# Kernel optimization log

Measured on AMD Instinct MI355X. Metric: run time of the kernel, lower is better.

The kernel has to match this reference:

```python
import jax, jax.numpy as jnp
import numpy as np

B, L, D_MODEL = 2, 2048, 256
D_STATE, D_CONV, EXPAND, HEADDIM = 128, 4, 4, 64
D_INNER = EXPAND * D_MODEL            # 1024
NHEADS = D_INNER // HEADDIM           # 16
CONV_DIM = D_INNER + 2 * D_STATE      # 1280
D_IN_PROJ = 2 * D_INNER + 2 * D_STATE + NHEADS  # 2320
CHUNK = 256
GN_EPS = float(np.finfo(np.float32).eps)
RMS_EPS = 1e-5


def _silu(x):
    return x * jax.nn.sigmoid(x)


def _segsum(x):
    # x: (..., T) -> (..., T, T); out[i, j] = sum_{j<k<=i} x[k] for i>=j else -inf
    T = x.shape[-1]
    cs = jnp.cumsum(x, -1)
    d = cs[..., :, None] - cs[..., None, :]
    mask = jnp.tril(jnp.ones((T, T), bool))
    return jnp.where(mask, d, -jnp.inf)


def _ssd(X, A, Bm, Cm):
    # Chunked SSD (Mamba2 ssd_minimal_discrete). X:(b,l,h,p) already dt-scaled,
    # A:(b,l,h) = dt * (-exp(A_log)), Bm/Cm:(b,l,n) with ngroups=1.
    b, l, h, p = X.shape
    c = l // CHUNK
    Xc = X.reshape(b, c, CHUNK, h, p)
    Ac = jnp.transpose(A.reshape(b, c, CHUNK, h), (0, 3, 1, 2))  # (b,h,c,Q)
    Bc = Bm.reshape(b, c, CHUNK, -1)
    Cc = Cm.reshape(b, c, CHUNK, -1)
    A_cs = jnp.cumsum(Ac, -1)                                    # (b,h,c,Q)
    Lmat = jnp.exp(_segsum(Ac))                                  # (b,h,c,Q,Q)
    CB = jnp.einsum('bcln,bcsn->bcls', Cc, Bc)                   # (b,c,Q,Q)
    Y_diag = jnp.einsum('bhcls,bcshp->bclhp', Lmat * CB[:, None], Xc)
    decay_states = jnp.exp(A_cs[..., -1:] - A_cs)                # (b,h,c,Q)
    states = jnp.einsum('bcln,bhcl,bclhp->bchpn', Bc, decay_states, Xc)
    states = jnp.concatenate([jnp.zeros_like(states[:, :1]), states], 1)  # (b,c+1,h,p,n)
    decay_chunk = jnp.exp(_segsum(jnp.pad(A_cs[..., -1], ((0, 0), (0, 0), (1, 0)))))  # (b,h,c+1,c+1)
    new_states = jnp.einsum('bhzc,bchpn->bzhpn', decay_chunk, states)[:, :-1]
    state_decay = jnp.exp(A_cs)                                  # (b,h,c,Q)
    Y_off = jnp.einsum('bcln,bchpn,bhcl->bclhp', Cc, new_states, state_decay)
    return (Y_diag + Y_off).reshape(b, l, h, p)


def _mamba2(u, in_w, conv_w, conv_b, dt_bias, A_log, Dh, norm_w, out_w):
    # u: (b, l, d_model)
    b, l, _ = u.shape
    zxbcdt = u @ in_w.T                                          # (b,l,D_IN_PROJ)
    z = zxbcdt[..., :D_INNER]
    xBC = zxbcdt[..., D_INNER:D_INNER + CONV_DIM]
    dt = jax.nn.softplus(zxbcdt[..., -NHEADS:] + dt_bias)        # (b,l,h)
    # causal depthwise conv over time
    xc = jnp.transpose(xBC, (0, 2, 1))                           # (b,C,l)
    xc = jax.lax.conv_general_dilated(xc, conv_w, (1,), [(D_CONV - 1, 0)],
                                      dimension_numbers=('NCH', 'OIH', 'NCH'),
                                      feature_group_count=CONV_DIM)
    xBC = _silu(jnp.transpose(xc + conv_b[None, :, None], (0, 2, 1)))
    x = xBC[..., :D_INNER].reshape(b, l, NHEADS, HEADDIM)
    Bm = xBC[..., D_INNER:D_INNER + D_STATE]
    Cm = xBC[..., D_INNER + D_STATE:]
    A = dt * (-jnp.exp(A_log))                                   # (b,l,h)
    y = _ssd(dt[..., None] * x, A, Bm, Cm) + x * Dh[None, None, :, None]
    y = y.reshape(b, l, D_INNER) * _silu(z)                      # gated
    y = y * jax.lax.rsqrt(jnp.mean(y * y, -1, keepdims=True) + RMS_EPS) * norm_w
    return y @ out_w.T                                           # (b,l,d_model)


def _resmamba(x, gn_w, gn_b, fp, bp, proj_w, proj_b):
    # GroupNorm(1, C) over (C, L) per sample
    mu = jnp.mean(x, (1, 2), keepdims=True)
    var = jnp.mean((x - mu) ** 2, (1, 2), keepdims=True)
    xn = (x - mu) * jax.lax.rsqrt(var + GN_EPS) * gn_w[None, :, None] + gn_b[None, :, None]
    t = jnp.transpose(xn, (0, 2, 1))                             # (B,L,C)
    fwd = _mamba2(t, *fp)
    bwd = jnp.flip(_mamba2(jnp.flip(t, 1), *bp), 1)
    r = jnp.concatenate([fwd + t, bwd + t], -1)                  # (B,L,2C)
    pr = r @ proj_w.T + proj_b                                   # (B,L,C)
    return x + jnp.transpose(pr, (0, 2, 1))


def setup_inputs():
    key = jax.random.key(0)
    ks = jax.random.split(key, 4)
    s = 0.02
    inp = {
        'x': jax.random.normal(ks[0], (B, D_MODEL, L), jnp.float32),
        'gn_w': jnp.ones((D_MODEL,), jnp.float32),
        'gn_b': jnp.zeros((D_MODEL,), jnp.float32),
        'proj_w': s * jax.random.normal(ks[1], (D_MODEL, 2 * D_MODEL), jnp.float32),
        'proj_b': jnp.zeros((D_MODEL,), jnp.float32),
    }
    for i, p in enumerate(('f', 'b')):
        kk = jax.random.split(ks[2 + i], 5)
        inp[p + '_in_w'] = s * jax.random.normal(kk[0], (D_IN_PROJ, D_MODEL), jnp.float32)
        inp[p + '_conv_w'] = s * jax.random.normal(kk[1], (CONV_DIM, 1, D_CONV), jnp.float32)
        inp[p + '_conv_b'] = jnp.zeros((CONV_DIM,), jnp.float32)
        inp[p + '_dt_bias'] = 0.1 * jax.random.normal(kk[2], (NHEADS,), jnp.float32)
        inp[p + '_A_log'] = jnp.log(jax.random.uniform(kk[3], (NHEADS,), jnp.float32, 1.0, 16.0))
        inp[p + '_D'] = jnp.ones((NHEADS,), jnp.float32)
        inp[p + '_norm_w'] = jnp.ones((D_INNER,), jnp.float32)
        inp[p + '_out_w'] = s * jax.random.normal(kk[4], (D_MODEL, D_INNER), jnp.float32)
    return inp


def reference(x, gn_w, gn_b, proj_w, proj_b,
              f_in_w, f_conv_w, f_conv_b, f_dt_bias, f_A_log, f_D, f_norm_w, f_out_w,
              b_in_w, b_conv_w, b_conv_b, b_dt_bias, b_A_log, b_D, b_norm_w, b_out_w):
    fp = (f_in_w, f_conv_w, f_conv_b, f_dt_bias, f_A_log, f_D, f_norm_w, f_out_w)
    bp = (b_in_w, b_conv_w, b_conv_b, b_dt_bias, b_A_log, b_D, b_norm_w, b_out_w)
    return _resmamba(x, gn_w, gn_b, fp, bp, proj_w, proj_b)
```

## Files before the change

### kernel.cpp

```cpp
#include <hip/hip_runtime.h>
#include <hip/hip_bf16.h>
#include <math.h>

using bf16 = __hip_bfloat16;

#define L_SEQ   2048
#define DMODEL  256
#define DINNER  1024
#define DSTATE  128
#define NH      16
#define HD      64
#define CONVDIM 1280
#define DPROJ   2320
#define NCHK    8
#define CT      256
#define BATCH   2
#define M_TOT   (BATCH*L_SEQ)

#define ACS_N   (BATCH*NH*NCHK*CT)
#define ST_N    ((size_t)BATCH*NCHK*NH*HD*DSTATE)
#define CB_N    ((size_t)BATCH*NCHK*CT*CT)

typedef __bf16 bf16x8_t __attribute__((ext_vector_type(8)));
typedef __bf16 bf16x4_t __attribute__((ext_vector_type(4)));
// ... 50 lines not shown
      for (int i = 0; i < 8; ++i) o[i] = tile[kr][j8+i];
      *(bf16x8_t*)&dst[(size_t)(k0+kr)*DMODEL + j0 + j8] = o;
    }
  } else if (bz < 1448){
    int i = ((bz - 1416)*256 + t)*8;
    int j = i & 255;
    const float* row = pw + (size_t)(i >> 8)*(2*DMODEL);
    bf16x8_t o;
    #pragma unroll
    for (int c = 0; c < 8; ++c) o[c] = (__bf16)(row[j+c] + row[256+j+c]);
    *(bf16x8_t*)&psum[i] = o;
  } else {
    int sub = bz - 1448;
    int blk = sub & 127, b = sub >> 7;
    const float4* p = (const float4*)(x + (size_t)b*(DMODEL*L_SEQ) + (size_t)blk*4096);
    float s = 0.f, ss = 0.f;
    #pragma unroll
    for (int k = 0; k < 4; ++k){
      float4 v = p[t + k*256];
      s  += v.x + v.y + v.z + v.w;
      ss += v.x*v.x + v.y*v.y + v.z*v.z + v.w*v.w;
    }
    for (int o = 32; o > 0; o >>= 1){ s += __shfl_down(s, o, 64); ss += __shfl_down(ss, o, 64); }
    if ((t & 63) == 0){ sh[(t>>6)*2] = s; sh[(t>>6)*2+1] = ss; }
    __syncthreads();
    if (t == 0){
      s  = sh[0]+sh[2]+sh[4]+sh[6];
      ss = sh[1]+sh[3]+sh[5]+sh[7];
      pbuf[b*128 + blk] = make_float2(s, ss);
    }
  }
}

__global__ __launch_bounds__(256) void k_t(const float* __restrict__ x, const float* __restrict__ gw,
                                           const float* __restrict__ gb, const float2* __restrict__ pbuf,
                                           bf16* __restrict__ t_out){
  __shared__ float tile[64][65];
  __shared__ float sh[4];
  int l0 = blockIdx.x*64, c0 = blockIdx.y*64, b = blockIdx.z;
  int tid = threadIdx.x;
  float s = 0.f, ss = 0.f;
  if (tid < 128){ float2 v = pbuf[b*128 + tid]; s = v.x; ss = v.y; }
  for (int o = 32; o > 0; o >>= 1){ s += __shfl_down(s, o, 64); ss += __shfl_down(ss, o, 64); }
  if (tid < 128 && (tid & 63) == 0){ sh[(tid>>6)*2] = s; sh[(tid>>6)*2+1] = ss; }
  __syncthreads();
  float inv = 1.f/(float)(DMODEL*L_SEQ);
  float s0 = sh[0]+sh[2], ss0 = sh[1]+sh[3];
  float mu = s0*inv, var = ss0*inv - mu*mu;
  float istd = rsqrtf(fmaxf(var, 0.f) + 1.1920929e-07f);

  int lx = tid & 63, cy = tid >> 6;
  for (int cc = cy; cc < 64; cc += 4){
    float v = x[(size_t)b*DMODEL*L_SEQ + (size_t)(c0+cc)*L_SEQ + l0+lx];
    tile[cc][lx] = (v - mu)*istd;
  }
  __syncthreads();
  int cx = tid & 63, ly = tid >> 6;
  float w = gw[c0+cx], bb = gb[c0+cx];
  for (int ll = ly; ll < 64; ll += 4)
    t_out[((size_t)(b*L_SEQ) + l0+ll)*DMODEL + c0+cx] = tob(tile[cx][ll]*w + bb);
}

__global__ __launch_bounds__(256) void gemm_inproj(const bf16* __restrict__ A, const bf16* __restrict__ B,
                                                   bf16* __restrict__ z, bf16* __restrict__ xbc,
                                                   float* __restrict__ dtb,
                                                   const float* __restrict__ db0, const float* __restrict__ db1){
  __shared__ __align__(16) bf16 lds[2][(128+128)*40];
  const int lda = DMODEL, ldb = DMODEL, N = DPROJ;
  int dir = blockIdx.z;
  const bf16* Bd = B + (size_t)dir*(size_t)N*ldb;
  int orig = blockIdx.x;
  int swz = (orig & 7)*76 + (orig >> 3);
  int m0 = (swz & 31)*128;
  int n0 = (swz >> 5)*128;
  int t = threadIdx.x;
  int wave = t >> 6, lane = t & 63;
  int wm = (wave & 1)*64, wn = (wave >> 1)*64;
  int lrow = lane & 15, quad = lane >> 4, lk8 = quad*8;

  int r0 = t >> 2, o0 = (t & 3)*8;
  int r1 = r0 + 64;
  int am0 = m0 + r0, am1 = m0 + r1;
  if (dir){
    am0 = (am0 & ~(L_SEQ-1)) | ((L_SEQ-1) - (am0 & (L_SEQ-1)));
    am1 = (am1 & ~(L_SEQ-1)) | ((L_SEQ-1) - (am1 & (L_SEQ-1)));
  }
  int bn0 = n0 + r0; if (bn0 > N-1) bn0 = N-1;
  int bn1 = n0 + r1; if (bn1 > N-1) bn1 = N-1;
  const bf16* Ap0 = A + (size_t)am0*lda + o0;
  const bf16* Ap1 = A + (size_t)am1*lda + o0;
  const bf16* Bp0 = Bd + (size_t)bn0*ldb + o0;
  const bf16* Bp1 = Bd + (size_t)bn1*ldb + o0;

  f32x4_t acc[4][4];
  #pragma unroll
  for (int i = 0; i < 4; ++i)
    #pragma unroll
    for (int j = 0; j < 4; ++j) acc[i][j] = (f32x4_t){0,0,0,0};

  int nit = 8;
  uint4 a0 = *(const uint4*)Ap0;
  uint4 a1 = *(const uint4*)Ap1;
  uint4 b0 = *(const uint4*)Bp0;
  uint4 b1 = *(const uint4*)Bp1;
  int st = 0;
  *(uint4*)&lds[0][r0*40 + o0] = a0;
  *(uint4*)&lds[0][r1*40 + o0] = a1;
  *(uint4*)&lds[0][(128 + r0)*40 + o0] = b0;
  *(uint4*)&lds[0][(128 + r1)*40 + o0] = b1;
  __syncthreads();
  for (int it = 0; it < nit; ++it){
    bool more = (it+1 < nit);
    if (more){
      int kk = (it+1) << 5;
      a0 = *(const uint4*)(Ap0 + kk);
      a1 = *(const uint4*)(Ap1 + kk);
      b0 = *(const uint4*)(Bp0 + kk);
      b1 = *(const uint4*)(Bp1 + kk);
    }
    const bf16* cs = lds[st];
    bf16x8_t bfr[4];
    #pragma unroll
    for (int ni = 0; ni < 4; ++ni) bfr[ni] = *(const bf16x8_t*)&cs[(128 + wn + ni*16 + lrow)*40 + lk8];
    #pragma unroll
    for (int mi = 0; mi < 4; ++mi){
      bf16x8_t af = *(const bf16x8_t*)&cs[(wm + mi*16 + lrow)*40 + lk8];
      #pragma unroll
      for (int ni = 0; ni < 4; ++ni)
        acc[mi][ni] = __builtin_amdgcn_mfma_f32_16x16x32_bf16(af, bfr[ni], acc[mi][ni], 0, 0, 0);
    }
    if (more){
      st ^= 1;
      *(uint4*)&lds[st][r0*40 + o0] = a0;
      *(uint4*)&lds[st][r1*40 + o0] = a1;
      *(uint4*)&lds[st][(128 + r0)*40 + o0] = b0;
      *(uint4*)&lds[st][(128 + r1)*40 + o0] = b1;
      __syncthreads();
    }
  }

  if (n0 < DINNER + CONVDIM){
    __syncthreads();
    __bf16* outs = (__bf16*)lds;
    #pragma unroll
    for (int mi = 0; mi < 4; ++mi)
      #pragma unroll
      for (int ni = 0; ni < 4; ++ni)
        #pragma unroll
        for (int r = 0; r < 4; ++r)
          outs[(wm + mi*16 + quad*4 + r)*132 + wn + ni*16 + lrow] = (__bf16)acc[mi][ni][r];
    __syncthreads();
    bf16* dst; int ldd, c0;
    if (n0 < DINNER){ dst = z   + (size_t)dir*M_TOT*DINNER;  ldd = DINNER;  c0 = n0; }
    else            { dst = xbc + (size_t)dir*M_TOT*CONVDIM; ldd = CONVDIM; c0 = n0 - DINNER; }
    #pragma unroll
    for (int itv = 0; itv < 8; ++itv){
      int v = t + itv*256;
      int row = v >> 4, cb = v & 15;
      *(bf16x8_t*)&dst[(size_t)(m0+row)*ldd + c0 + cb*8] =
          *(const bf16x8_t*)&outs[row*132 + cb*8];
    }
  } else {
    const float* db = dir ? db1 : db0;
    float* dtp = dtb + (size_t)dir*((size_t)M_TOT*NH);
    #pragma unroll
    for (int mi = 0; mi < 4; ++mi)
      #pragma unroll
      for (int ni = 0; ni < 4; ++ni)
        #pragma unroll
        for (int r = 0; r < 4; ++r){
          int m = m0 + wm + mi*16 + quad*4 + r;
          int n = n0 + wn + ni*16 + lrow;
          if (n < N){
            int h = n - (DINNER + CONVDIM);
            float xx = acc[mi][ni][r] + db[h];
            dtp[(size_t)m*NH + h] = (xx > 20.f) ? xx : log1pf(expf(xx));
          }
        }
  }
}

__global__ __launch_bounds__(256) void gemm_w(const bf16* __restrict__ P, const bf16* __restrict__ owt,
                                              bf16* __restrict__ W){
  __shared__ __align__(16) bf16 lds[2][(128+64)*40];
  int dir = blockIdx.z;
  int m0 = blockIdx.x*128, n0 = blockIdx.y*64;
  int t = threadIdx.x;
  int wave = t >> 6, lane = t & 63;
  int wm = (wave & 1)*64, wn = (wave >> 1)*32;
  int lrow = lane & 15, quad = lane >> 4, lk8 = quad*8;

  int r0 = t >> 2, o0 = (t & 3)*8;
  int r1 = r0 + 64;
  const bf16* Ap0 = P + (size_t)(m0 + r0)*(2*DMODEL) + dir*DMODEL + o0;
  const bf16* Ap1 = P + (size_t)(m0 + r1)*(2*DMODEL) + dir*DMODEL + o0;
  const bf16* Bp  = owt + (size_t)dir*DINNER*DMODEL + (size_t)(n0 + r0)*DMODEL + o0;

  f32x4_t acc[4][2];
  #pragma unroll
  for (int i = 0; i < 4; ++i){ acc[i][0] = (f32x4_t){0,0,0,0}; acc[i][1] = (f32x4_t){0,0,0,0}; }

  int nit = DMODEL >> 5;
  uint4 a0 = *(const uint4*)Ap0;
  uint4 a1 = *(const uint4*)Ap1;
  uint4 b0 = *(const uint4*)Bp;
  int st = 0;
  *(uint4*)&lds[0][r0*40 + o0] = a0;
  *(uint4*)&lds[0][r1*40 + o0] = a1;
  *(uint4*)&lds[0][(128 + r0)*40 + o0] = b0;
  __syncthreads();
  for (int it = 0; it < nit; ++it){
    bool more = (it+1 < nit);
    if (more){
      int kk = (it+1) << 5;
      a0 = *(const uint4*)(Ap0 + kk);
      a1 = *(const uint4*)(Ap1 + kk);
      b0 = *(const uint4*)(Bp + kk);
    }
    const bf16* cs = lds[st];
    bf16x8_t af[4], bfr[2];
    #pragma unroll
    for (int mi = 0; mi < 4; ++mi) af[mi] = *(const bf16x8_t*)&cs[(wm + mi*16 + lrow)*40 + lk8];
    #pragma unroll
    for (int ni = 0; ni < 2; ++ni) bfr[ni] = *(const bf16x8_t*)&cs[(128 + wn + ni*16 + lrow)*40 + lk8];
    #pragma unroll
    for (int mi = 0; mi < 4; ++mi)
      #pragma unroll
      for (int ni = 0; ni < 2; ++ni)
        acc[mi][ni] = __builtin_amdgcn_mfma_f32_16x16x32_bf16(af[mi], bfr[ni], acc[mi][ni], 0, 0, 0);
    if (more){
      st ^= 1;
      *(uint4*)&lds[st][r0*40 + o0] = a0;
      *(uint4*)&lds[st][r1*40 + o0] = a1;
      *(uint4*)&lds[st][(128 + r0)*40 + o0] = b0;
      __syncthreads();
    }
  }
  bf16* Wd = W + (size_t)dir*DMODEL*DINNER;
  #pragma unroll
  for (int mi = 0; mi < 4; ++mi)
    #pragma unroll
    for (int ni = 0; ni < 2; ++ni)
      #pragma unroll
      for (int r = 0; r < 4; ++r){
        int m = m0 + wm + mi*16 + quad*4 + r;
        int n = n0 + wn + ni*16 + lrow;
        Wd[(size_t)m*DINNER + n] = tob(acc[mi][ni][r]);
      }
}

__global__ __launch_bounds__(256) void gemm_final(const bf16* __restrict__ y, const bf16* __restrict__ tb,
                                                  const bf16* __restrict__ W, const bf16* __restrict__ psum,
                                                  const float* __restrict__ x, const float* __restrict__ pb,
                                                  float* __restrict__ out){
  __shared__ __align__(16) bf16 lds[2][(32+64)*72];
  __shared__ float tile[32][65];
  int orig = blockIdx.x;
  int swz = (orig & 7)*64 + (orig >> 3);
  int mt_ = swz & 127, nt_ = swz >> 7;
  int m0 = mt_*32, n0 = nt_*64;
  int t = threadIdx.x;
  int wave = t >> 6, lane = t & 63;
  int lrow = lane & 15, quad = lane >> 4, lk8 = quad*8;
  int wn = wave*16;

  f32x4_t acc[2];
  acc[0] = (f32x4_t){0,0,0,0}; acc[1] = (f32x4_t){0,0,0,0};

  int rowA = t >> 3, oA = (t & 7)*8;
  int rowB0 = t >> 3, oB0 = (t & 7)*8;
  int rowB1 = (t + 256) >> 3, oB1 = (t & 7)*8;

  #pragma unroll
  for (int ph = 0; ph < 3; ++ph){
    const bf16 *Ab, *Bb; int lda, ldb, K, rev;
    if (ph == 0){ Ab = y;                             lda = DINNER; K = DINNER; Bb = W;                             ldb = DINNER; rev = 0; }
    else if (ph == 1){ Ab = y + (size_t)M_TOT*DINNER; lda = DINNER; K = DINNER; Bb = W + (size_t)DMODEL*DINNER;     ldb = DINNER; rev = 1; }
    else { Ab = tb; lda = DMODEL; K = DMODEL; Bb = psum; ldb = DMODEL; rev = 0; }

    int am = m0 + rowA;
    if (rev) am = (am & ~(L_SEQ-1)) | ((L_SEQ-1) - (am & (L_SEQ-1)));
// ... 89 lines not shown
  {
    float4 b0v = *(const float4*)&cb[ch0];
    float4 b1v = *(const float4*)&cb[ch0+4];
    bias[0]=b0v.x; bias[1]=b0v.y; bias[2]=b0v.z; bias[3]=b0v.w;
    bias[4]=b1v.x; bias[5]=b1v.y; bias[6]=b1v.z; bias[7]=b1v.w;
  }

  bf16x8_t zero;
  #pragma unroll
  for (int c = 0; c < 8; ++c) zero[c] = (__bf16)0.f;

  bf16x8_t win[4];
  #pragma unroll
  for (int k = 0; k < 3; ++k){
    int ls = lbase - 3 + k;
    win[k] = (ls >= 0) ? *(const bf16x8_t*)&xr[(size_t)ls*CONVDIM] : zero;
  }
  #pragma unroll
  for (int i = 0; i < 4; ++i){
    int l = lbase + i;
    win[3] = *(const bf16x8_t*)&xr[(size_t)l*CONVDIM];
    bf16x8_t outv;
    #pragma unroll
    for (int c = 0; c < 8; ++c){
      float a = bias[c] + (float)win[0][c]*wk[0][c] + (float)win[1][c]*wk[1][c]
                        + (float)win[2][c]*wk[2][c] + (float)win[3][c]*wk[3][c];
      outv[c] = (__bf16)(a / (1.f + __expf(-a)));
    }
    *(bf16x8_t*)&xcv[(size_t)l*CONVDIM] = outv;
    win[0] = win[1]; win[1] = win[2]; win[2] = win[3];
  }
}

__global__ __launch_bounds__(256) void k_states(const bf16* __restrict__ xconv, const float* __restrict__ dt,
                                                const float* __restrict__ Al0, const float* __restrict__ Al1,
                                                float* __restrict__ A_cs, float* __restrict__ states){
  int id0 = blockIdx.x;
  int dir = id0 >> 8; int id = id0 & 255;
  int h = id & 15; int bc = id >> 4; int ch = bc & 7; int b = bc >> 3;
  int t = threadIdx.x;
  __shared__ float s_acs[CT];
  __shared__ float w_s[CT];
  __shared__ __align__(16) __bf16 Xt[64*72];
  __shared__ __align__(16) __bf16 Bt[128*72];
  const bf16* xc = xconv + (size_t)dir*((size_t)M_TOT*CONVDIM);
  const float* dtp = dt + (size_t)dir*((size_t)M_TOT*NH);
  const float* Alog = dir ? Al1 : Al0;
  size_t rowbase = (size_t)(b*L_SEQ) + ch*CT;

  float dtv = dtp[(rowbase + t)*NH + h];
  s_acs[t] = -expf(Alog[h]) * dtv;
  __syncthreads();
  for (int off = 1; off < 256; off <<= 1){
    float v = (t >= off) ? s_acs[t-off] : 0.f;
    __syncthreads();
    s_acs[t] += v;
    __syncthreads();
  }
  A_cs[(size_t)dir*ACS_N + (size_t)((b*NH+h)*NCHK + ch)*CT + t] = s_acs[t];
  float alast = s_acs[CT-1];
  w_s[t] = dtv * __expf(fminf(alast - s_acs[t], 0.f));
  __syncthreads();

  int wave = t >> 6, lane = t & 63, lrow = lane & 15, quad = lane >> 4;
  f32x4_t acc[8];
  #pragma unroll
  for (int i = 0; i < 8; ++i) acc[i] = (f32x4_t){0.f,0.f,0.f,0.f};

  for (int kt = 0; kt < 4; ++kt){
    int l0 = kt*64;
    #pragma unroll
    for (int it = 0; it < 2; ++it){
      int idx = t + it*256; int l = idx >> 3; int p0 = (idx & 7)*8;
      bf16x8_t v = *(const bf16x8_t*)&xc[(rowbase + l0 + l)*CONVDIM + h*HD + p0];
      float w = w_s[l0 + l];
      int col = (((l>>3) ^ ((p0>>3)&7))<<3) | (l&7);
      #pragma unroll
      for (int j = 0; j < 8; ++j) Xt[(p0+j)*72 + col] = (__bf16)((float)v[j]*w);
    }
    #pragma unroll
    for (int it = 0; it < 4; ++it){
      int idx = t + it*256; int l = idx >> 4; int n0 = (idx & 15)*8;
      bf16x8_t v = *(const bf16x8_t*)&xc[(rowbase + l0 + l)*CONVDIM + DINNER + n0];
      int col = (((l>>3) ^ ((n0>>3)&7))<<3) | (l&7);
      #pragma unroll
      for (int j = 0; j < 8; ++j) Bt[(n0+j)*72 + col] = v[j];
    }
    __syncthreads();
    int arow = wave*16 + lrow;
    #pragma unroll
    for (int ks = 0; ks < 2; ++ks){
      int kg = ks*4 + quad;
      bf16x8_t af = *(const bf16x8_t*)&Xt[arow*72 + ((kg ^ ((arow>>3)&7))<<3)];
      #pragma unroll
      for (int nt = 0; nt < 8; ++nt){
        int brow = nt*16 + lrow;
        bf16x8_t bq = *(const bf16x8_t*)&Bt[brow*72 + ((kg ^ ((brow>>3)&7))<<3)];
        acc[nt] = __builtin_amdgcn_mfma_f32_16x16x32_bf16(af, bq, acc[nt], 0, 0, 0);
      }
    }
    __syncthreads();
  }
  float* so = states + (size_t)dir*ST_N + (size_t)id*HD*DSTATE;
  int m = wave*16 + quad*4;
  #pragma unroll
  for (int nt = 0; nt < 8; ++nt)
    #pragma unroll
    for (int r = 0; r < 4; ++r)
      so[(size_t)(m+r)*DSTATE + nt*16 + lrow] = acc[nt][r];
}

__global__ __launch_bounds__(256) void k_recur(const float* __restrict__ states, bf16* __restrict__ nsb,
                                               const float* __restrict__ A_cs){
  int blk = blockIdx.x;
  int bh2 = blk >> 5;
  int e = (blk & 31)*256 + threadIdx.x;
  int dir = bh2 >> 5; int bh = bh2 & 31;
  int h = bh & 15, b = bh >> 4;
  const float* ac = A_cs + (size_t)dir*ACS_N;
  const float* st = states + (size_t)dir*ST_N;
  bf16* nb = nsb + (size_t)dir*ST_N;
  float s = 0.f;
  #pragma unroll
  for (int ch = 0; ch < NCHK; ++ch){
    float dec = expdec(ac[((size_t)(bh*NCHK+ch))*CT + CT-1]);
    size_t off = (size_t)(((b*NCHK+ch)*NH)+h)*HD*DSTATE + e;
    float cur = st[off];
    nb[off] = tob(s);
    s = s*dec + cur;
  }
}

__global__ __launch_bounds__(256) void k_cb(const bf16* __restrict__ xconv, bf16* __restrict__ CB){
  int zz = blockIdx.z;
  int dir = zz >> 4; int b = (zz >> 3) & 1; int ch = zz & 7;
  int m0 = blockIdx.x*64, n0 = blockIdx.y*64;
  if (n0 > m0) return;
  const bf16* base = xconv + (size_t)dir*((size_t)M_TOT*CONVDIM) + (size_t)(b*L_SEQ + ch*CT)*CONVDIM;
  const bf16* Crow = base + DINNER + DSTATE;
  const bf16* Brow = base + DINNER;
  __shared__ __align__(16) __bf16 As[64*136];
  __shared__ __align__(16) __bf16 Bs[64*136];
  int t = threadIdx.x;
  int r = t >> 2, o0 = (t & 3)*32;
  #pragma unroll
  for (int j = 0; j < 4; ++j){
    *(bf16x8_t*)&As[r*136 + o0 + j*8] = *(const bf16x8_t*)&Crow[(size_t)(m0+r)*CONVDIM + o0 + j*8];
    *(bf16x8_t*)&Bs[r*136 + o0 + j*8] = *(const bf16x8_t*)&Brow[(size_t)(n0+r)*CONVDIM + o0 + j*8];
  }
  __syncthreads();
  int wave = t >> 6, lane = t & 63, lrow = lane & 15, quad = lane >> 4;
  int wm = wave*16;
  f32x4_t acc[4];
  #pragma unroll
  for (int i = 0; i < 4; ++i) acc[i] = (f32x4_t){0.f,0.f,0.f,0.f};
  #pragma unroll
  for (int ks = 0; ks < 4; ++ks){
    bf16x8_t af = *(const bf16x8_t*)&As[(wm+lrow)*136 + ks*32 + quad*8];
    #pragma unroll
    for (int nt = 0; nt < 4; ++nt){
      bf16x8_t bq = *(const bf16x8_t*)&Bs[(nt*16+lrow)*136 + ks*32 + quad*8];
      acc[nt] = __builtin_amdgcn_mfma_f32_16x16x32_bf16(af, bq, acc[nt], 0, 0, 0);
    }
  }
  __syncthreads();
  #pragma unroll
  for (int nt = 0; nt < 4; ++nt)
    #pragma unroll
    for (int r2 = 0; r2 < 4; ++r2)
      As[(wm + quad*4 + r2)*72 + nt*16 + lrow] = (__bf16)acc[nt][r2];
  __syncthreads();
  bf16* outp = CB + (size_t)dir*CB_N + (size_t)(b*NCHK+ch)*CT*CT;
  #pragma unroll
  for (int p = 0; p < 2; ++p){
    int idx = t + p*256;
    int row = idx >> 3, c8 = (idx & 7)*8;
    *(bf16x8_t*)&outp[(size_t)(m0+row)*CT + n0 + c8] = *(const bf16x8_t*)&As[row*72 + c8];
  }
}

__global__ __launch_bounds__(512) void k_y_mfma(const bf16* __restrict__ xconv, const float* __restrict__ dt,
                                                const float* __restrict__ A_cs, const bf16* __restrict__ CB,
                                                const bf16* __restrict__ ns, bf16* __restrict__ y){
  int id0 = blockIdx.x;
  int dir = id0 >> 8; int id = id0 & 255;
  int h = id & 15; int bc = id >> 4; int ch = bc & 7; int b = bc >> 3;
  int t = threadIdx.x;
  int lane = t & 63;
  int lrow = lane & 15, quad = lane >> 4;

  __shared__ __align__(16) bf16 Xs[64*264];
  __shared__ __align__(16) bf16 NSs[64*136];
  __shared__ float acs_s[CT];

  const bf16* xc = xconv + (size_t)dir*((size_t)M_TOT*CONVDIM);
  const float* dtp = dt + (size_t)dir*((size_t)M_TOT*NH);
  const float* acs = A_cs + (size_t)dir*ACS_N + (size_t)((b*NH+h)*NCHK + ch)*CT;
  const bf16* cbz = CB + (size_t)dir*CB_N + (size_t)(b*NCHK+ch)*CT*CT;
  const bf16* nsp = ns + (size_t)dir*ST_N + (size_t)(((b*NCHK+ch)*NH)+h)*HD*DSTATE;
  bf16* yp = y + (size_t)dir*((size_t)M_TOT*DINNER);
  size_t rowbase = (size_t)(b*L_SEQ + ch*CT);
  if (t < CT) acs_s[t] = acs[t];

  #pragma unroll
  for (int it = 0; it < 4; ++it){
    int idx = t + it*512;
    int s = idx >> 3, p0 = (idx & 7)*8;
    float dtv = dtp[(rowbase + s)*NH + h];
    bf16x8_t v = *(const bf16x8_t*)&xc[(rowbase + s)*CONVDIM + h*HD + p0];
    int col = ((((s>>3) ^ ((p0>>3)&7)))<<3) | (s&7);
// ... 140 lines not shown
  (void)in_sizes; (void)n_in; (void)out_size; (void)ws_size;
  const float* x      = (const float*)d_in[0];
  const float* gn_w   = (const float*)d_in[1];
  const float* gn_b   = (const float*)d_in[2];
  const float* proj_w = (const float*)d_in[3];
  const float* proj_b = (const float*)d_in[4];
  float* out = (float*)d_out;

  char* wp = (char*)d_ws;
  auto alloc = [&](size_t bytes){ void* r = (void*)wp; wp += (bytes + 255) & ~(size_t)255; return r; };
  bf16*  t_buf  = (bf16*) alloc((size_t)M_TOT*DMODEL*2);
  bf16*  z_buf  = (bf16*) alloc((size_t)2*M_TOT*DINNER*2);
  bf16*  xraw   = (bf16*) alloc((size_t)2*M_TOT*CONVDIM*2);
  bf16*  xconv  = (bf16*) alloc((size_t)2*M_TOT*CONVDIM*2);
  float* dt_buf = (float*)alloc((size_t)2*M_TOT*NH*4);
  float* acs    = (float*)alloc((size_t)2*ACS_N*4);
  float* states = (float*)alloc((size_t)2*ST_N*4);
  bf16*  nsb    = (bf16*) alloc((size_t)2*ST_N*2);
  bf16*  cb     = (bf16*) alloc((size_t)2*CB_N*2);
  float2* pbuf  = (float2*)alloc(BATCH*128*sizeof(float2));
  bf16*  inw_bf   = (bf16*)alloc((size_t)2*DPROJ*DMODEL*2);
  bf16*  projw_bf = (bf16*)alloc((size_t)DMODEL*2*DMODEL*2);
  bf16*  owt      = (bf16*)alloc((size_t)2*DINNER*DMODEL*2);
  bf16*  wfb      = (bf16*)alloc((size_t)2*DMODEL*DINNER*2);
  bf16*  psum     = (bf16*)alloc((size_t)DMODEL*DMODEL*2);
  bf16*  y_buf    = xraw;

  k_front<<<1704, 256, 0, stream>>>(
      (const float*)d_in[5], (const float*)d_in[13], proj_w,
      inw_bf, projw_bf,
      (const float*)d_in[12], (const float*)d_in[20], owt, psum,
      x, pbuf);

  gemm_w<<<dim3(2, 16, 2), 256, 0, stream>>>(projw_bf, owt, wfb);

  k_t<<<dim3(32,4,2), 256, 0, stream>>>(x, gn_w, gn_b, pbuf, t_buf);

  gemm_inproj<<<dim3(608, 1, 2), 256, 0, stream>>>(
      t_buf, inw_bf, z_buf, xraw, dt_buf,
      (const float*)d_in[8], (const float*)d_in[16]);

  k_conv<<<dim3(5, L_SEQ/32, 2*BATCH), 256, 0, stream>>>(
      xraw, (const float*)d_in[6], (const float*)d_in[7],
            (const float*)d_in[14], (const float*)d_in[15], xconv);
  k_states<<<2*BATCH*NCHK*NH, 256, 0, stream>>>(
      xconv, dt_buf, (const float*)d_in[9], (const float*)d_in[17], acs, states);
  k_recur<<<2*BATCH*NH*32, 256, 0, stream>>>(states, nsb, acs);
  k_cb<<<dim3(4,4,2*BATCH*NCHK), 256, 0, stream>>>(xconv, cb);
  k_y_mfma<<<2*BATCH*NCHK*NH, 512, 0, stream>>>(xconv, dt_buf, acs, cb, nsb, y_buf);
  k_gaterms<<<2*M_TOT, 256, 0, stream>>>(
      z_buf, (const float*)d_in[11], (const float*)d_in[19], xconv,
      (const float*)d_in[10], (const float*)d_in[18], y_buf);

  gemm_final<<<512, 256, 0, stream>>>(y_buf, t_buf, wfb, psum, x, proj_b, out);
}
```

Baseline: 220.8 us.

## Merge independent kernels into combined launches and widen in-proj GEMM blocks

Merges gemm_w and k_t into one launch that branches on block index, and merges k_states and k_cb into another, so independent work shares a launch and fills the GPU better. The k_cb part now runs before k_recur instead of after it. gemm_inproj moves to 512 threads per block, with each wave computing a 64x32 sub-tile and each thread loading one row instead of two. This cuts launch count and per-thread register pressure, at the cost of a larger shared-memory footprint in the fused kernels and some idle early-exit blocks.

```diff
diff --git a/kernel.cpp b/kernel.cpp
--- a/kernel.cpp
+++ b/kernel.cpp
@@ -106,36 +106,108 @@
   }
 }
 
-__global__ __launch_bounds__(256) void k_t(const float* __restrict__ x, const float* __restrict__ gw,
-                                           const float* __restrict__ gb, const float2* __restrict__ pbuf,
-                                           bf16* __restrict__ t_out){
+__global__ __launch_bounds__(256) void k_wt(const bf16* __restrict__ P, const bf16* __restrict__ owt,
+                                            bf16* __restrict__ W,
+                                            const float* __restrict__ x, const float* __restrict__ gw,
+                                            const float* __restrict__ gb, const float2* __restrict__ pbuf,
+                                            bf16* __restrict__ t_out){
+  __shared__ __align__(16) bf16 lds[2][(128+64)*40];
   __shared__ float tile[64][65];
   __shared__ float sh[4];
-  int l0 = blockIdx.x*64, c0 = blockIdx.y*64, b = blockIdx.z;
-  int tid = threadIdx.x;
-  float s = 0.f, ss = 0.f;
-  if (tid < 128){ float2 v = pbuf[b*128 + tid]; s = v.x; ss = v.y; }
-  for (int o = 32; o > 0; o >>= 1){ s += __shfl_down(s, o, 64); ss += __shfl_down(ss, o, 64); }
-  if (tid < 128 && (tid & 63) == 0){ sh[(tid>>6)*2] = s; sh[(tid>>6)*2+1] = ss; }
-  __syncthreads();
-  float inv = 1.f/(float)(DMODEL*L_SEQ);
-  float s0 = sh[0]+sh[2], ss0 = sh[1]+sh[3];
-  float mu = s0*inv, var = ss0*inv - mu*mu;
-  float istd = rsqrtf(fmaxf(var, 0.f) + 1.1920929e-07f);
-
-  int lx = tid & 63, cy = tid >> 6;
-  for (int cc = cy; cc < 64; cc += 4){
-    float v = x[(size_t)b*DMODEL*L_SEQ + (size_t)(c0+cc)*L_SEQ + l0+lx];
-    tile[cc][lx] = (v - mu)*istd;
-  }
-  __syncthreads();
-  int cx = tid & 63, ly = tid >> 6;
-  float w = gw[c0+cx], bb = gb[c0+cx];
-  for (int ll = ly; ll < 64; ll += 4)
-    t_out[((size_t)(b*L_SEQ) + l0+ll)*DMODEL + c0+cx] = tob(tile[cx][ll]*w + bb);
-}
-
-__global__ __launch_bounds__(256) void gemm_inproj(const bf16* __restrict__ A, const bf16* __restrict__ B,
+  int bz6 = blockIdx.x;
+  int t = threadIdx.x;
+  if (bz6 < 64){
+    int dir = bz6 & 1;
+    int m0 = (bz6 >> 5)*128, n0 = ((bz6 >> 1) & 15)*64;
+    int wave = t >> 6, lane = t & 63;
+    int wm = (wave & 1)*64, wn = (wave >> 1)*32;
+    int lrow = lane & 15, quad = lane >> 4, lk8 = quad*8;
+
+    int r0 = t >> 2, o0 = (t & 3)*8;
+    int r1 = r0 + 64;
+    const bf16* Ap0 = P + (size_t)(m0 + r0)*(2*DMODEL) + dir*DMODEL + o0;
+    const bf16* Ap1 = P + (size_t)(m0 + r1)*(2*DMODEL) + dir*DMODEL + o0;
+    const bf16* Bp  = owt + (size_t)dir*DINNER*DMODEL + (size_t)(n0 + r0)*DMODEL + o0;
+
+    f32x4_t acc[4][2];
+    #pragma unroll
+    for (int i = 0; i < 4; ++i){ acc[i][0] = (f32x4_t){0,0,0,0}; acc[i][1] = (f32x4_t){0,0,0,0}; }
+
+    int nit = DMODEL >> 5;
+    uint4 a0 = *(const uint4*)Ap0;
+    uint4 a1 = *(const uint4*)Ap1;
+    uint4 b0 = *(const uint4*)Bp;
+    int st = 0;
+    *(uint4*)&lds[0][r0*40 + o0] = a0;
+    *(uint4*)&lds[0][r1*40 + o0] = a1;
+    *(uint4*)&lds[0][(128 + r0)*40 + o0] = b0;
+    __syncthreads();
+    for (int it = 0; it < nit; ++it){
+      bool more = (it+1 < nit);
+      if (more){
+        int kk = (it+1) << 5;
+        a0 = *(const uint4*)(Ap0 + kk);
+        a1 = *(const uint4*)(Ap1 + kk);
+        b0 = *(const uint4*)(Bp + kk);
+      }
+      const bf16* cs = lds[st];
+      bf16x8_t af[4], bfr[2];
+      #pragma unroll
+      for (int mi = 0; mi < 4; ++mi) af[mi] = *(const bf16x8_t*)&cs[(wm + mi*16 + lrow)*40 + lk8];
+      #pragma unroll
+      for (int ni = 0; ni < 2; ++ni) bfr[ni] = *(const bf16x8_t*)&cs[(128 + wn + ni*16 + lrow)*40 + lk8];
+      #pragma unroll
+      for (int mi = 0; mi < 4; ++mi)
+        #pragma unroll
+        for (int ni = 0; ni < 2; ++ni)
+          acc[mi][ni] = __builtin_amdgcn_mfma_f32_16x16x32_bf16(af[mi], bfr[ni], acc[mi][ni], 0, 0, 0);
+      if (more){
+        st ^= 1;
+        *(uint4*)&lds[st][r0*40 + o0] = a0;
+        *(uint4*)&lds[st][r1*40 + o0] = a1;
+        *(uint4*)&lds[st][(128 + r0)*40 + o0] = b0;
+        __syncthreads();
+      }
+    }
+    bf16* Wd = W + (size_t)dir*DMODEL*DINNER;
+    #pragma unroll
+    for (int mi = 0; mi < 4; ++mi)
+      #pragma unroll
+      for (int ni = 0; ni < 2; ++ni)
+        #pragma unroll
+        for (int r = 0; r < 4; ++r){
+          int m = m0 + wm + mi*16 + quad*4 + r;
+          int n = n0 + wn + ni*16 + lrow;
+          Wd[(size_t)m*DINNER + n] = tob(acc[mi][ni][r]);
+        }
+  } else {
+    int sub = bz6 - 64;
+    int l0 = (sub & 31)*64, c0 = ((sub >> 5) & 3)*64, b = sub >> 7;
+    int tid = t;
+    float s = 0.f, ss = 0.f;
+    if (tid < 128){ float2 v = pbuf[b*128 + tid]; s = v.x; ss = v.y; }
+    for (int o = 32; o > 0; o >>= 1){ s += __shfl_down(s, o, 64); ss += __shfl_down(ss, o, 64); }
+    if (tid < 128 && (tid & 63) == 0){ sh[(tid>>6)*2] = s; sh[(tid>>6)*2+1] = ss; }
+    __syncthreads();
+    float inv = 1.f/(float)(DMODEL*L_SEQ);
+    float s0 = sh[0]+sh[2], ss0 = sh[1]+sh[3];
+    float mu = s0*inv, var = ss0*inv - mu*mu;
+    float istd = rsqrtf(fmaxf(var, 0.f) + 1.1920929e-07f);
+
+    int lx = tid & 63, cy = tid >> 6;
+    for (int cc = cy; cc < 64; cc += 4){
+      float v = x[(size_t)b*DMODEL*L_SEQ + (size_t)(c0+cc)*L_SEQ + l0+lx];
+      tile[cc][lx] = (v - mu)*istd;
+    }
+    __syncthreads();
+    int cx = tid & 63, ly = tid >> 6;
+    float w = gw[c0+cx], bb = gb[c0+cx];
+    for (int ll = ly; ll < 64; ll += 4)
+      t_out[((size_t)(b*L_SEQ) + l0+ll)*DMODEL + c0+cx] = tob(tile[cx][ll]*w + bb);
+  }
+}
+
+__global__ __launch_bounds__(512) void gemm_inproj(const bf16* __restrict__ A, const bf16* __restrict__ B,
                                                    bf16* __restrict__ z, bf16* __restrict__ xbc,
                                                    float* __restrict__ dtb,
                                                    const float* __restrict__ db0, const float* __restrict__ db1){
@@ -149,66 +221,49 @@
   int n0 = (swz >> 5)*128;
   int t = threadIdx.x;
   int wave = t >> 6, lane = t & 63;
-  int wm = (wave & 1)*64, wn = (wave >> 1)*64;
+  int wm = (wave & 1)*64, wn = (wave >> 1)*32;
   int lrow = lane & 15, quad = lane >> 4, lk8 = quad*8;
 
-  int r0 = t >> 2, o0 = (t & 3)*8;
-  int r1 = r0 + 64;
-  int am0 = m0 + r0, am1 = m0 + r1;
-  if (dir){
-    am0 = (am0 & ~(L_SEQ-1)) | ((L_SEQ-1) - (am0 & (L_SEQ-1)));
-    am1 = (am1 & ~(L_SEQ-1)) | ((L_SEQ-1) - (am1 & (L_SEQ-1)));
-  }
-  int bn0 = n0 + r0; if (bn0 > N-1) bn0 = N-1;
-  int bn1 = n0 + r1; if (bn1 > N-1) bn1 = N-1;
-  const bf16* Ap0 = A + (size_t)am0*lda + o0;
-  const bf16* Ap1 = A + (size_t)am1*lda + o0;
-  const bf16* Bp0 = Bd + (size_t)bn0*ldb + o0;
-  const bf16* Bp1 = Bd + (size_t)bn1*ldb + o0;
-
-  f32x4_t acc[4][4];
-  #pragma unroll
-  for (int i = 0; i < 4; ++i)
-    #pragma unroll
-    for (int j = 0; j < 4; ++j) acc[i][j] = (f32x4_t){0,0,0,0};
+  int rA = t >> 2, oA = (t & 3)*8;
+  int amA = m0 + rA;
+  if (dir) amA = (amA & ~(L_SEQ-1)) | ((L_SEQ-1) - (amA & (L_SEQ-1)));
+  int bnA = n0 + rA; if (bnA > N-1) bnA = N-1;
+  const bf16* Ap = A + (size_t)amA*lda + oA;
+  const bf16* Bp = Bd + (size_t)bnA*ldb + oA;
+
+  f32x4_t acc[4][2];
+  #pragma unroll
+  for (int i = 0; i < 4; ++i){ acc[i][0] = (f32x4_t){0,0,0,0}; acc[i][1] = (f32x4_t){0,0,0,0}; }
 
   int nit = 8;
-  uint4 a0 = *(const uint4*)Ap0;
-  uint4 a1 = *(const uint4*)Ap1;
-  uint4 b0 = *(const uint4*)Bp0;
-  uint4 b1 = *(const uint4*)Bp1;
+  uint4 a0 = *(const uint4*)Ap;
+  uint4 b0 = *(const uint4*)Bp;
   int st = 0;
-  *(uint4*)&lds[0][r0*40 + o0] = a0;
-  *(uint4*)&lds[0][r1*40 + o0] = a1;
-  *(uint4*)&lds[0][(128 + r0)*40 + o0] = b0;
-  *(uint4*)&lds[0][(128 + r1)*40 + o0] = b1;
+  *(uint4*)&lds[0][rA*40 + oA] = a0;
+  *(uint4*)&lds[0][(128 + rA)*40 + oA] = b0;
   __syncthreads();
   for (int it = 0; it < nit; ++it){
     bool more = (it+1 < nit);
     if (more){
       int kk = (it+1) << 5;
-      a0 = *(const uint4*)(Ap0 + kk);
-      a1 = *(const uint4*)(Ap1 + kk);
-      b0 = *(const uint4*)(Bp0 + kk);
-      b1 = *(const uint4*)(Bp1 + kk);
+      a0 = *(const uint4*)(Ap + kk);
+      b0 = *(const uint4*)(Bp + kk);
     }
     const bf16* cs = lds[st];
-    bf16x8_t bfr[4];
-    #pragma unroll
-    for (int ni = 0; ni < 4; ++ni) bfr[ni] = *(const bf16x8_t*)&cs[(128 + wn + ni*16 + lrow)*40 + lk8];
+    bf16x8_t bfr[2];
+    #pragma unroll
+    for (int ni = 0; ni < 2; ++ni) bfr[ni] = *(const bf16x8_t*)&cs[(128 + wn + ni*16 + lrow)*40 + lk8];
     #pragma unroll
     for (int mi = 0; mi < 4; ++mi){
       bf16x8_t af = *(const bf16x8_t*)&cs[(wm + mi*16 + lrow)*40 + lk8];
       #pragma unroll
-      for (int ni = 0; ni < 4; ++ni)
+      for (int ni = 0; ni < 2; ++ni)
         acc[mi][ni] = __builtin_amdgcn_mfma_f32_16x16x32_bf16(af, bfr[ni], acc[mi][ni], 0, 0, 0);
     }
     if (more){
       st ^= 1;
-      *(uint4*)&lds[st][r0*40 + o0] = a0;
-      *(uint4*)&lds[st][r1*40 + o0] = a1;
-      *(uint4*)&lds[st][(128 + r0)*40 + o0] = b0;
-      *(uint4*)&lds[st][(128 + r1)*40 + o0] = b1;
+      *(uint4*)&lds[st][rA*40 + oA] = a0;
+      *(uint4*)&lds[st][(128 + rA)*40 + oA] = b0;
       __syncthreads();
     }
   }
@@ -219,7 +274,7 @@
     #pragma unroll
     for (int mi = 0; mi < 4; ++mi)
       #pragma unroll
-      for (int ni = 0; ni < 4; ++ni)
+      for (int ni = 0; ni < 2; ++ni)
         #pragma unroll
         for (int r = 0; r < 4; ++r)
           outs[(wm + mi*16 + quad*4 + r)*132 + wn + ni*16 + lrow] = (__bf16)acc[mi][ni][r];
@@ -228,8 +283,8 @@
     if (n0 < DINNER){ dst = z   + (size_t)dir*M_TOT*DINNER;  ldd = DINNER;  c0 = n0; }
     else            { dst = xbc + (size_t)dir*M_TOT*CONVDIM; ldd = CONVDIM; c0 = n0 - DINNER; }
     #pragma unroll
-    for (int itv = 0; itv < 8; ++itv){
-      int v = t + itv*256;
+    for (int itv = 0; itv < 4; ++itv){
+      int v = t + itv*512;
       int row = v >> 4, cb = v & 15;
       *(bf16x8_t*)&dst[(size_t)(m0+row)*ldd + c0 + cb*8] =
           *(const bf16x8_t*)&outs[row*132 + cb*8];
@@ -240,7 +295,7 @@
     #pragma unroll
     for (int mi = 0; mi < 4; ++mi)
       #pragma unroll
-      for (int ni = 0; ni < 4; ++ni)
+      for (int ni = 0; ni < 2; ++ni)
         #pragma unroll
         for (int r = 0; r < 4; ++r){
           int m = m0 + wm + mi*16 + quad*4 + r;
@@ -252,75 +307,6 @@
           }
         }
   }
-}
-
-__global__ __launch_bounds__(256) void gemm_w(const bf16* __restrict__ P, const bf16* __restrict__ owt,
-                                              bf16* __restrict__ W){
-  __shared__ __align__(16) bf16 lds[2][(128+64)*40];
-  int dir = blockIdx.z;
-  int m0 = blockIdx.x*128, n0 = blockIdx.y*64;
-  int t = threadIdx.x;
-  int wave = t >> 6, lane = t & 63;
-  int wm = (wave & 1)*64, wn = (wave >> 1)*32;
-  int lrow = lane & 15, quad = lane >> 4, lk8 = quad*8;
-
-  int r0 = t >> 2, o0 = (t & 3)*8;
-  int r1 = r0 + 64;
-  const bf16* Ap0 = P + (size_t)(m0 + r0)*(2*DMODEL) + dir*DMODEL + o0;
-  const bf16* Ap1 = P + (size_t)(m0 + r1)*(2*DMODEL) + dir*DMODEL + o0;
-  const bf16* Bp  = owt + (size_t)dir*DINNER*DMODEL + (size_t)(n0 + r0)*DMODEL + o0;
-
-  f32x4_t acc[4][2];
-  #pragma unroll
-  for (int i = 0; i < 4; ++i){ acc[i][0] = (f32x4_t){0,0,0,0}; acc[i][1] = (f32x4_t){0,0,0,0}; }
-
-  int nit = DMODEL >> 5;
-  uint4 a0 = *(const uint4*)Ap0;
-  uint4 a1 = *(const uint4*)Ap1;
-  uint4 b0 = *(const uint4*)Bp;
-  int st = 0;
-  *(uint4*)&lds[0][r0*40 + o0] = a0;
-  *(uint4*)&lds[0][r1*40 + o0] = a1;
-  *(uint4*)&lds[0][(128 + r0)*40 + o0] = b0;
-  __syncthreads();
-  for (int it = 0; it < nit; ++it){
-    bool more = (it+1 < nit);
-    if (more){
-      int kk = (it+1) << 5;
-      a0 = *(const uint4*)(Ap0 + kk);
-      a1 = *(const uint4*)(Ap1 + kk);
-      b0 = *(const uint4*)(Bp + kk);
-    }
-    const bf16* cs = lds[st];
-    bf16x8_t af[4], bfr[2];
-    #pragma unroll
-    for (int mi = 0; mi < 4; ++mi) af[mi] = *(const bf16x8_t*)&cs[(wm + mi*16 + lrow)*40 + lk8];
-    #pragma unroll
-    for (int ni = 0; ni < 2; ++ni) bfr[ni] = *(const bf16x8_t*)&cs[(128 + wn + ni*16 + lrow)*40 + lk8];
-    #pragma unroll
-    for (int mi = 0; mi < 4; ++mi)
-      #pragma unroll
-      for (int ni = 0; ni < 2; ++ni)
-        acc[mi][ni] = __builtin_amdgcn_mfma_f32_16x16x32_bf16(af[mi], bfr[ni], acc[mi][ni], 0, 0, 0);
-    if (more){
-      st ^= 1;
-      *(uint4*)&lds[st][r0*40 + o0] = a0;
-      *(uint4*)&lds[st][r1*40 + o0] = a1;
-      *(uint4*)&lds[st][(128 + r0)*40 + o0] = b0;
-      __syncthreads();
-    }
-  }
-  bf16* Wd = W + (size_t)dir*DMODEL*DINNER;
-  #pragma unroll
-  for (int mi = 0; mi < 4; ++mi)
-    #pragma unroll
-    for (int ni = 0; ni < 2; ++ni)
-      #pragma unroll
-      for (int r = 0; r < 4; ++r){
-        int m = m0 + wm + mi*16 + quad*4 + r;
-        int n = n0 + wn + ni*16 + lrow;
-        Wd[(size_t)m*DINNER + n] = tob(acc[mi][ni][r]);
-      }
 }
 
 __global__ __launch_bounds__(256) void gemm_final(const bf16* __restrict__ y, const bf16* __restrict__ tb,
@@ -476,82 +462,133 @@
   }
 }
 
-__global__ __launch_bounds__(256) void k_states(const bf16* __restrict__ xconv, const float* __restrict__ dt,
-                                                const float* __restrict__ Al0, const float* __restrict__ Al1,
-                                                float* __restrict__ A_cs, float* __restrict__ states){
-  int id0 = blockIdx.x;
-  int dir = id0 >> 8; int id = id0 & 255;
-  int h = id & 15; int bc = id >> 4; int ch = bc & 7; int b = bc >> 3;
-  int t = threadIdx.x;
-  __shared__ float s_acs[CT];
-  __shared__ float w_s[CT];
-  __shared__ __align__(16) __bf16 Xt[64*72];
-  __shared__ __align__(16) __bf16 Bt[128*72];
-  const bf16* xc = xconv + (size_t)dir*((size_t)M_TOT*CONVDIM);
-  const float* dtp = dt + (size_t)dir*((size_t)M_TOT*NH);
-  const float* Alog = dir ? Al1 : Al0;
-  size_t rowbase = (size_t)(b*L_SEQ) + ch*CT;
-
-  float dtv = dtp[(rowbase + t)*NH + h];
-  s_acs[t] = -expf(Alog[h]) * dtv;
-  __syncthreads();
-  for (int off = 1; off < 256; off <<= 1){
-    float v = (t >= off) ? s_acs[t-off] : 0.f;
-    __syncthreads();
-    s_acs[t] += v;
-    __syncthreads();
-  }
-  A_cs[(size_t)dir*ACS_N + (size_t)((b*NH+h)*NCHK + ch)*CT + t] = s_acs[t];
-  float alast = s_acs[CT-1];
-  w_s[t] = dtv * __expf(fminf(alast - s_acs[t], 0.f));
-  __syncthreads();
-
-  int wave = t >> 6, lane = t & 63, lrow = lane & 15, quad = lane >> 4;
-  f32x4_t acc[8];
-  #pragma unroll
-  for (int i = 0; i < 8; ++i) acc[i] = (f32x4_t){0.f,0.f,0.f,0.f};
-
-  for (int kt = 0; kt < 4; ++kt){
-    int l0 = kt*64;
-    #pragma unroll
-    for (int it = 0; it < 2; ++it){
-      int idx = t + it*256; int l = idx >> 3; int p0 = (idx & 7)*8;
-      bf16x8_t v = *(const bf16x8_t*)&xc[(rowbase + l0 + l)*CONVDIM + h*HD + p0];
-      float w = w_s[l0 + l];
-      int col = (((l>>3) ^ ((p0>>3)&7))<<3) | (l&7);
-      #pragma unroll
-      for (int j = 0; j < 8; ++j) Xt[(p0+j)*72 + col] = (__bf16)((float)v[j]*w);
-    }
-    #pragma unroll
-    for (int it = 0; it < 4; ++it){
-      int idx = t + it*256; int l = idx >> 4; int n0 = (idx & 15)*8;
-      bf16x8_t v = *(const bf16x8_t*)&xc[(rowbase + l0 + l)*CONVDIM + DINNER + n0];
-      int col = (((l>>3) ^ ((n0>>3)&7))<<3) | (l&7);
-      #pragma unroll
-      for (int j = 0; j < 8; ++j) Bt[(n0+j)*72 + col] = v[j];
-    }
-    __syncthreads();
-    int arow = wave*16 + lrow;
-    #pragma unroll
-    for (int ks = 0; ks < 2; ++ks){
-      int kg = ks*4 + quad;
-      bf16x8_t af = *(const bf16x8_t*)&Xt[arow*72 + ((kg ^ ((arow>>3)&7))<<3)];
-      #pragma unroll
-      for (int nt = 0; nt < 8; ++nt){
-        int brow = nt*16 + lrow;
-        bf16x8_t bq = *(const bf16x8_t*)&Bt[brow*72 + ((kg ^ ((brow>>3)&7))<<3)];
+__global__ __launch_bounds__(256) void k_states_cb(const bf16* __restrict__ xconv, const float* __restrict__ dt,
+                                                   const float* __restrict__ Al0, const float* __restrict__ Al1,
+                                                   float* __restrict__ A_cs, float* __restrict__ states,
+                                                   bf16* __restrict__ CB){
+  __shared__ __align__(16) char smem[34816];
+  int bz = blockIdx.x, t = threadIdx.x;
+  if (bz < 512){
+    float* s_acs = (float*)smem;
+    float* w_s   = (float*)(smem + 1024);
+    __bf16* Xt   = (__bf16*)(smem + 2048);
+    __bf16* Bt   = (__bf16*)(smem + 2048 + 9216);
+    int id0 = bz;
+    int dir = id0 >> 8; int id = id0 & 255;
+    int h = id & 15; int bc = id >> 4; int ch = bc & 7; int b = bc >> 3;
+    const bf16* xc = xconv + (size_t)dir*((size_t)M_TOT*CONVDIM);
+    const float* dtp = dt + (size_t)dir*((size_t)M_TOT*NH);
+    const float* Alog = dir ? Al1 : Al0;
+    size_t rowbase = (size_t)(b*L_SEQ) + ch*CT;
+
+    float dtv = dtp[(rowbase + t)*NH + h];
+    s_acs[t] = -expf(Alog[h]) * dtv;
+    __syncthreads();
+    for (int off = 1; off < 256; off <<= 1){
+      float v = (t >= off) ? s_acs[t-off] : 0.f;
+      __syncthreads();
+      s_acs[t] += v;
+      __syncthreads();
+    }
+    A_cs[(size_t)dir*ACS_N + (size_t)((b*NH+h)*NCHK + ch)*CT + t] = s_acs[t];
+    float alast = s_acs[CT-1];
+    w_s[t] = dtv * __expf(fminf(alast - s_acs[t], 0.f));
+    __syncthreads();
+
+    int wave = t >> 6, lane = t & 63, lrow = lane & 15, quad = lane >> 4;
+    f32x4_t acc[8];
+    #pragma unroll
+    for (int i = 0; i < 8; ++i) acc[i] = (f32x4_t){0.f,0.f,0.f,0.f};
+
+    for (int kt = 0; kt < 4; ++kt){
+      int l0 = kt*64;
+      #pragma unroll
+      for (int it = 0; it < 2; ++it){
+        int idx = t + it*256; int l = idx >> 3; int p0 = (idx & 7)*8;
+        bf16x8_t v = *(const bf16x8_t*)&xc[(rowbase + l0 + l)*CONVDIM + h*HD + p0];
+        float w = w_s[l0 + l];
+        int col = (((l>>3) ^ ((p0>>3)&7))<<3) | (l&7);
+        #pragma unroll
+        for (int j = 0; j < 8; ++j) Xt[(p0+j)*72 + col] = (__bf16)((float)v[j]*w);
+      }
+      #pragma unroll
+      for (int it = 0; it < 4; ++it){
+        int idx = t + it*256; int l = idx >> 4; int n0 = (idx & 15)*8;
+        bf16x8_t v = *(const bf16x8_t*)&xc[(rowbase + l0 + l)*CONVDIM + DINNER + n0];
+        int col = (((l>>3) ^ ((n0>>3)&7))<<3) | (l&7);
+        #pragma unroll
+        for (int j = 0; j < 8; ++j) Bt[(n0+j)*72 + col] = v[j];
+      }
+      __syncthreads();
+      int arow = wave*16 + lrow;
+      #pragma unroll
+      for (int ks = 0; ks < 2; ++ks){
+        int kg = ks*4 + quad;
+        bf16x8_t af = *(const bf16x8_t*)&Xt[arow*72 + ((kg ^ ((arow>>3)&7))<<3)];
+        #pragma unroll
+        for (int nt = 0; nt < 8; ++nt){
+          int brow = nt*16 + lrow;
+          bf16x8_t bq = *(const bf16x8_t*)&Bt[brow*72 + ((kg ^ ((brow>>3)&7))<<3)];
+          acc[nt] = __builtin_amdgcn_mfma_f32_16x16x32_bf16(af, bq, acc[nt], 0, 0, 0);
+        }
+      }
+      __syncthreads();
+    }
+    float* so = states + (size_t)dir*ST_N + (size_t)id*HD*DSTATE;
+    int m = wave*16 + quad*4;
+    #pragma unroll
+    for (int nt = 0; nt < 8; ++nt)
+      #pragma unroll
+      for (int r = 0; r < 4; ++r)
+        so[(size_t)(m+r)*DSTATE + nt*16 + lrow] = acc[nt][r];
+  } else {
+    __bf16* As = (__bf16*)smem;
+    __bf16* Bs = (__bf16*)(smem + 17408);
+    int sub = bz - 512;
+    int zz = sub >> 4;
+    int dir = zz >> 4; int b = (zz >> 3) & 1; int ch = zz & 7;
+    int rest = sub & 15;
+    int m0 = (rest >> 2)*64, n0 = (rest & 3)*64;
+    if (n0 > m0) return;
+    const bf16* base = xconv + (size_t)dir*((size_t)M_TOT*CONVDIM) + (size_t)(b*L_SEQ + ch*CT)*CONVDIM;
+    const bf16* Crow = base + DINNER + DSTATE;
+    const bf16* Brow = base + DINNER;
+    int r = t >> 2, o0 = (t & 3)*32;
+    #pragma unroll
+    for (int j = 0; j < 4; ++j){
+      *(bf16x8_t*)&As[r*136 + o0 + j*8] = *(const bf16x8_t*)&Crow[(size_t)(m0+r)*CONVDIM + o0 + j*8];
+      *(bf16x8_t*)&Bs[r*136 + o0 + j*8] = *(const bf16x8_t*)&Brow[(size_t)(n0+r)*CONVDIM + o0 + j*8];
+    }
+    __syncthreads();
+    int wave = t >> 6, lane = t & 63, lrow = lane & 15, quad = lane >> 4;
+    int wm = wave*16;
+    f32x4_t acc[4];
+    #pragma unroll
+    for (int i = 0; i < 4; ++i) acc[i] = (f32x4_t){0.f,0.f,0.f,0.f};
+    #pragma unroll
+    for (int ks = 0; ks < 4; ++ks){
+      bf16x8_t af = *(const bf16x8_t*)&As[(wm+lrow)*136 + ks*32 + quad*8];
+      #pragma unroll
+      for (int nt = 0; nt < 4; ++nt){
+        bf16x8_t bq = *(const bf16x8_t*)&Bs[(nt*16+lrow)*136 + ks*32 + quad*8];
         acc[nt] = __builtin_amdgcn_mfma_f32_16x16x32_bf16(af, bq, acc[nt], 0, 0, 0);
       }
     }
     __syncthreads();
-  }
-  float* so = states + (size_t)dir*ST_N + (size_t)id*HD*DSTATE;
-  int m = wave*16 + quad*4;
-  #pragma unroll
-  for (int nt = 0; nt < 8; ++nt)
-    #pragma unroll
-    for (int r = 0; r < 4; ++r)
-      so[(size_t)(m+r)*DSTATE + nt*16 + lrow] = acc[nt][r];
+    #pragma unroll
+    for (int nt = 0; nt < 4; ++nt)
+      #pragma unroll
+      for (int r2 = 0; r2 < 4; ++r2)
+        As[(wm + quad*4 + r2)*72 + nt*16 + lrow] = (__bf16)acc[nt][r2];
+    __syncthreads();
+    bf16* outp = CB + (size_t)dir*CB_N + (size_t)(b*NCHK+ch)*CT*CT;
+    #pragma unroll
+    for (int p = 0; p < 2; ++p){
+      int idx = t + p*256;
+      int row = idx >> 3, c8 = (idx & 7)*8;
+      *(bf16x8_t*)&outp[(size_t)(m0+row)*CT + n0 + c8] = *(const bf16x8_t*)&As[row*72 + c8];
+    }
+  }
 }
 
 __global__ __launch_bounds__(256) void k_recur(const float* __restrict__ states, bf16* __restrict__ nsb,
@@ -572,54 +609,6 @@
     float cur = st[off];
     nb[off] = tob(s);
     s = s*dec + cur;
-  }
-}
-
-__global__ __launch_bounds__(256) void k_cb(const bf16* __restrict__ xconv, bf16* __restrict__ CB){
-  int zz = blockIdx.z;
-  int dir = zz >> 4; int b = (zz >> 3) & 1; int ch = zz & 7;
-  int m0 = blockIdx.x*64, n0 = blockIdx.y*64;
-  if (n0 > m0) return;
-  const bf16* base = xconv + (size_t)dir*((size_t)M_TOT*CONVDIM) + (size_t)(b*L_SEQ + ch*CT)*CONVDIM;
-  const bf16* Crow = base + DINNER + DSTATE;
-  const bf16* Brow = base + DINNER;
-  __shared__ __align__(16) __bf16 As[64*136];
-  __shared__ __align__(16) __bf16 Bs[64*136];
-  int t = threadIdx.x;
-  int r = t >> 2, o0 = (t & 3)*32;
-  #pragma unroll
-  for (int j = 0; j < 4; ++j){
-    *(bf16x8_t*)&As[r*136 + o0 + j*8] = *(const bf16x8_t*)&Crow[(size_t)(m0+r)*CONVDIM + o0 + j*8];
-    *(bf16x8_t*)&Bs[r*136 + o0 + j*8] = *(const bf16x8_t*)&Brow[(size_t)(n0+r)*CONVDIM + o0 + j*8];
-  }
-  __syncthreads();
-  int wave = t >> 6, lane = t & 63, lrow = lane & 15, quad = lane >> 4;
-  int wm = wave*16;
-  f32x4_t acc[4];
-  #pragma unroll
-  for (int i = 0; i < 4; ++i) acc[i] = (f32x4_t){0.f,0.f,0.f,0.f};
-  #pragma unroll
-  for (int ks = 0; ks < 4; ++ks){
-    bf16x8_t af = *(const bf16x8_t*)&As[(wm+lrow)*136 + ks*32 + quad*8];
-    #pragma unroll
-    for (int nt = 0; nt < 4; ++nt){
-      bf16x8_t bq = *(const bf16x8_t*)&Bs[(nt*16+lrow)*136 + ks*32 + quad*8];
-      acc[nt] = __builtin_amdgcn_mfma_f32_16x16x32_bf16(af, bq, acc[nt], 0, 0, 0);
-    }
-  }
-  __syncthreads();
-  #pragma unroll
-  for (int nt = 0; nt < 4; ++nt)
-    #pragma unroll
-    for (int r2 = 0; r2 < 4; ++r2)
-      As[(wm + quad*4 + r2)*72 + nt*16 + lrow] = (__bf16)acc[nt][r2];
-  __syncthreads();
-  bf16* outp = CB + (size_t)dir*CB_N + (size_t)(b*NCHK+ch)*CT*CT;
-  #pragma unroll
-  for (int p = 0; p < 2; ++p){
-    int idx = t + p*256;
-    int row = idx >> 3, c8 = (idx & 7)*8;
-    *(bf16x8_t*)&outp[(size_t)(m0+row)*CT + n0 + c8] = *(const bf16x8_t*)&As[row*72 + c8];
   }
 }
 
@@ -826,21 +815,18 @@
       (const float*)d_in[12], (const float*)d_in[20], owt, psum,
       x, pbuf);
 
-  gemm_w<<<dim3(2, 16, 2), 256, 0, stream>>>(projw_bf, owt, wfb);
-
-  k_t<<<dim3(32,4,2), 256, 0, stream>>>(x, gn_w, gn_b, pbuf, t_buf);
-
-  gemm_inproj<<<dim3(608, 1, 2), 256, 0, stream>>>(
+  k_wt<<<320, 256, 0, stream>>>(projw_bf, owt, wfb, x, gn_w, gn_b, pbuf, t_buf);
+
+  gemm_inproj<<<dim3(608, 1, 2), 512, 0, stream>>>(
       t_buf, inw_bf, z_buf, xraw, dt_buf,
       (const float*)d_in[8], (const float*)d_in[16]);
 
   k_conv<<<dim3(5, L_SEQ/32, 2*BATCH), 256, 0, stream>>>(
       xraw, (const float*)d_in[6], (const float*)d_in[7],
             (const float*)d_in[14], (const float*)d_in[15], xconv);
-  k_states<<<2*BATCH*NCHK*NH, 256, 0, stream>>>(
-      xconv, dt_buf, (const float*)d_in[9], (const float*)d_in[17], acs, states);
+  k_states_cb<<<1024, 256, 0, stream>>>(
+      xconv, dt_buf, (const float*)d_in[9], (const float*)d_in[17], acs, states, cb);
   k_recur<<<2*BATCH*NH*32, 256, 0, stream>>>(states, nsb, acs);
-  k_cb<<<dim3(4,4,2*BATCH*NCHK), 256, 0, stream>>>(xconv, cb);
   k_y_mfma<<<2*BATCH*NCHK*NH, 512, 0, stream>>>(xconv, dt_buf, acs, cb, nsb, y_buf);
   k_gaterms<<<2*M_TOT, 256, 0, stream>>>(
       z_buf, (const float*)d_in[11], (const float*)d_in[19], xconv,
```

Result: faster. 207.2 us (median of 2 runs) (-6.2%).
